# Kernel tuning notes

Hardware: AMD Instinct MI355X
Metric: run time of the kernel (lower is better)

Reference implementation:

```python
import jax, jax.numpy as jnp
import numpy as np

IOU_THRESHOLD = 0.5


def setup_inputs() -> dict:
    key = jax.random.key(0)
    k_xy, k_wh, k_jit, k_cls, k_lab = jax.random.split(key, 5)
    B, P, T, C = 16, 16384, 128, 80
    # valid x1y1x2y2 ground-truth boxes in [0,1]
    xy = jax.random.uniform(k_xy, (B, T, 2), dtype=jnp.float32) * 0.7
    wh = jax.random.uniform(k_wh, (B, T, 2), dtype=jnp.float32) * 0.25 + 0.05
    true_bboxes = jnp.concatenate([xy, xy + wh], axis=-1)  # [B,T,4]
    # predictions: tiled GT boxes + small jitter so many pairs exceed IoU 0.5
    reps = P // T
    base = jnp.tile(true_bboxes, (1, reps, 1))  # [B,P,4]
    pred_bboxes = base + 0.02 * jax.random.normal(k_jit, (B, P, 4), dtype=jnp.float32)
    pred_classes = jax.random.normal(k_cls, (B, P, C), dtype=jnp.float32)
    true_labels = jax.random.randint(k_lab, (B, T), 0, C, dtype=jnp.int64)
    return {
        "pred_bboxes": pred_bboxes,
        "pred_classes": pred_classes,
        "true_bboxes": true_bboxes,
        "true_labels": true_labels,
    }


def _iou_matrix(pred, true):
    # pred [B,P,4], true [B,T,4] -> [B,P,T]
    p = pred[:, :, None, :]  # [B,P,1,4]
    t = true[:, None, :, :]  # [B,1,T,4]
    x1 = jnp.maximum(p[..., 0], t[..., 0])
    y1 = jnp.maximum(p[..., 1], t[..., 1])
    x2 = jnp.minimum(p[..., 2], t[..., 2])
    y2 = jnp.minimum(p[..., 3], t[..., 3])
    inter = jnp.clip(x2 - x1, 0.0) * jnp.clip(y2 - y1, 0.0)
    pa = (pred[..., 2] - pred[..., 0]) * (pred[..., 3] - pred[..., 1])  # [B,P]
    ta = (true[..., 2] - true[..., 0]) * (true[..., 3] - true[..., 1])  # [B,T]
    union = pa[:, :, None] + ta[:, None, :] - inter
    return inter / union


def _smooth_l1(d):
    ad = jnp.abs(d)
    return jnp.where(ad < 1.0, 0.5 * d * d, ad - 0.5)


def reference(pred_bboxes, pred_classes, true_bboxes, true_labels):
    B, P, _ = pred_bboxes.shape
    iou = _iou_matrix(pred_bboxes, true_bboxes)          # [B,P,T]
    max_iou = jnp.max(iou, axis=2)                       # [B,P]
    max_idx = jnp.argmax(iou, axis=2)                    # [B,P]
    matched_true = jnp.take_along_axis(
        true_bboxes, jnp.broadcast_to(max_idx[:, :, None], (B, P, 4)), axis=1
    )                                                    # [B,P,4]
    mask = (max_iou > IOU_THRESHOLD).astype(pred_bboxes.dtype)  # [B,P]
    elem = _smooth_l1(pred_bboxes - matched_true)        # [B,P,4]
    n_matched = jnp.sum(mask)
    bbox_loss = jnp.sum(elem * mask[:, :, None]) / jnp.maximum(4.0 * n_matched, 1.0)
    # classification: per image, first prediction's logits vs first GT label
    logits = pred_classes[:, 0, :]                       # [B,C]
    labels = true_labels[:, 0]                           # [B]
    logp = jax.nn.log_softmax(logits, axis=-1)
    cls_loss = -jnp.mean(jnp.take_along_axis(logp, labels[:, None], axis=1))
    return bbox_loss + cls_loss
```

## Files before the change

kernel.cpp:

```cpp
#include <hip/hip_runtime.h>
#include <hip/hip_bf16.h>
#include <math.h>

#define B_ 16
#define P_ 16384
#define T_ 128
#define C_ 80


__device__ __forceinline__ float smooth_l1(float d) {
    float ad = fabsf(d);
    return (ad < 1.0f) ? 0.5f * d * d : ad - 0.5f;
}

__global__ __launch_bounds__(256) void det_loss_main(
        const float* __restrict__ pred_bboxes,
        const float* __restrict__ true_bboxes,
        float* __restrict__ ws)
{
    const int blocks_per_b = P_ / 512;
    const int b    = blockIdx.x / blocks_per_b;
    const int pblk = blockIdx.x % blocks_per_b;
    const int tid  = threadIdx.x;

    __shared__ float4 tb[T_];
    if (tid < T_) tb[tid] = ((const float4*)true_bboxes)[b * T_ + tid];
    __syncthreads();

    const float4* pbase = (const float4*)pred_bboxes + (size_t)b * P_ + pblk * 512;
    const float4 pA = pbase[tid];
    const float4 pB = pbase[tid + 256];
    const float paA = (pA.z - pA.x) * (pA.w - pA.y);
    const float paB = (pB.z - pB.x) * (pB.w - pB.y);

    float biA = 0.0f, buA = 1.0f; int bxA = 0;
    float biB = 0.0f, buB = 1.0f; int bxB = 0;

    #pragma unroll 8
    for (int t = 0; t < T_; ++t) {
        const float4 t4 = tb[t];
        const float ta = (t4.z - t4.x) * (t4.w - t4.y);

        {
            const float iw = fmaxf(fminf(pA.z, t4.z) - fmaxf(pA.x, t4.x), 0.0f);
            const float ih = fmaxf(fminf(pA.w, t4.w) - fmaxf(pA.y, t4.y), 0.0f);
            const float inter = iw * ih;
            const float u = (paA + ta) - inter;
            const bool upd = inter * buA > biA * u;
            biA = upd ? inter : biA;
            buA = upd ? u : buA;
            bxA = upd ? t : bxA;
        }
        {
            const float iw = fmaxf(fminf(pB.z, t4.z) - fmaxf(pB.x, t4.x), 0.0f);
            const float ih = fmaxf(fminf(pB.w, t4.w) - fmaxf(pB.y, t4.y), 0.0f);
            const float inter = iw * ih;
            const float u = (paB + ta) - inter;
            const bool upd = inter * buB > biB * u;
            biB = upd ? inter : biB;
            buB = upd ? u : buB;
            bxB = upd ? t : bxB;
        }
    }

    float contrib = 0.0f, cnt = 0.0f;
    if (2.0f * biA > buA) {
        const float4 m4 = tb[bxA];
        contrib += smooth_l1(pA.x - m4.x) + smooth_l1(pA.y - m4.y)
                 + smooth_l1(pA.z - m4.z) + smooth_l1(pA.w - m4.w);
        cnt += 1.0f;
    }
    if (2.0f * biB > buB) {
        const float4 m4 = tb[bxB];
        contrib += smooth_l1(pB.x - m4.x) + smooth_l1(pB.y - m4.y)
                 + smooth_l1(pB.z - m4.z) + smooth_l1(pB.w - m4.w);
        cnt += 1.0f;
    }

    #pragma unroll
    for (int off = 32; off > 0; off >>= 1) {
        contrib += __shfl_down(contrib, off, 64);
        cnt     += __shfl_down(cnt,     off, 64);
    }
    __shared__ float sc[4], sn[4];
    const int wave = tid >> 6, lane = tid & 63;
    if (lane == 0) { sc[wave] = contrib; sn[wave] = cnt; }
    __syncthreads();
    if (tid == 0) {
        ws[blockIdx.x]       = sc[0] + sc[1] + sc[2] + sc[3];
        ws[512 + blockIdx.x] = sn[0] + sn[1] + sn[2] + sn[3];
    }
}

__global__ __launch_bounds__(1024) void det_loss_final(
        const float* __restrict__ pred_classes,
        const int*   __restrict__ true_labels,
        const float* __restrict__ ws,
        float* __restrict__ out)
{
    const int tid = threadIdx.x;
    const int wave = tid >> 6, lane = tid & 63;

    __shared__ float rowloss[B_];
    __shared__ float wc[16], wn[16];

    const float* row = pred_classes + (size_t)wave * P_ * C_;
    const float v0 = row[lane];
    const float v1 = (lane < C_ - 64) ? row[lane + 64] : -INFINITY;
    float m = fmaxf(v0, v1);
    #pragma unroll
    for (int off = 32; off > 0; off >>= 1) m = fmaxf(m, __shfl_xor(m, off, 64));
    float s = expf(v0 - m) + ((lane < C_ - 64) ? expf(v1 - m) : 0.0f);
    #pragma unroll
    for (int off = 32; off > 0; off >>= 1) s += __shfl_xor(s, off, 64);
    if (lane == 0) {
        const int lab = true_labels[wave * T_];
        rowloss[wave] = -(row[lab] - m - logf(s));
    }

    float sc = 0.0f, sn = 0.0f;
    if (tid < 128) {
        const float4 c4 = ((const float4*)ws)[tid];
        const float4 n4 = ((const float4*)(ws + 512))[tid];
        sc = c4.x + c4.y + c4.z + c4.w;
        sn = n4.x + n4.y + n4.z + n4.w;
    }
    #pragma unroll
    for (int off = 32; off > 0; off >>= 1) {
        sc += __shfl_down(sc, off, 64);
        sn += __shfl_down(sn, off, 64);
    }
    if (lane == 0) { wc[wave] = sc; wn[wave] = sn; }
    __syncthreads();

    if (tid == 0) {
        float C = 0.0f, N = 0.0f, cl = 0.0f;
        #pragma unroll
        for (int w = 0; w < 16; ++w) { C += wc[w]; N += wn[w]; cl += rowloss[w]; }
        out[0] = C / fmaxf(4.0f * N, 1.0f) + cl * (1.0f / B_);
    }
}

extern "C" void kernel_launch(void* const* d_in, const int* in_sizes, int n_in,
                              void* d_out, int out_size, void* d_ws, size_t ws_size,
                              hipStream_t stream) {
    const float* pred_bboxes  = (const float*)d_in[0];
    const float* pred_classes = (const float*)d_in[1];
    const float* true_bboxes  = (const float*)d_in[2];
    const int*   true_labels  = (const int*)d_in[3];
    float* out = (float*)d_out;
    float* ws  = (float*)d_ws;

    det_loss_main<<<B_ * (P_ / 512), 256, 0, stream>>>(pred_bboxes, true_bboxes, ws);
    det_loss_final<<<1, 1024, 0, stream>>>(pred_classes, true_labels, ws, out);
}
```

Before: 133.5 us.

## Fuse final reduction into main kernel via last-block atomic counter

Merges the two kernels into one. A global atomic counter lets the last finishing block do the final reduction, and the classification log-softmax moves into one wave of each image's first block. Ground-truth boxes are now read straight from global memory as scalar loads instead of being staged in LDS. The IoU comparison now tracks pa+ta instead of the union, with the threshold rewritten as 3*inter > sum. This removes a kernel launch and one LDS barrier, at the cost of a memset launch and an atomic/threadfence per block.

Result: slower. 141.3 us (+5.9%).

```diff
diff --git a/kernel.cpp b/kernel.cpp
--- a/kernel.cpp
+++ b/kernel.cpp
@@ -6,6 +6,7 @@
 #define P_ 16384
 #define T_ 128
 #define C_ 80
+#define NBLK 512
 
 
 __device__ __forceinline__ float smooth_l1(float d) {
@@ -13,19 +14,20 @@
     return (ad < 1.0f) ? 0.5f * d * d : ad - 0.5f;
 }
 
-__global__ __launch_bounds__(256) void det_loss_main(
+__global__ __launch_bounds__(256) void det_loss_fused(
         const float* __restrict__ pred_bboxes,
+        const float* __restrict__ pred_classes,
         const float* __restrict__ true_bboxes,
-        float* __restrict__ ws)
+        const int*   __restrict__ true_labels,
+        float* __restrict__ ws,
+        float* __restrict__ out)
 {
-    const int blocks_per_b = P_ / 512;
-    const int b    = blockIdx.x / blocks_per_b;
-    const int pblk = blockIdx.x % blocks_per_b;
     const int tid  = threadIdx.x;
+    const int b    = blockIdx.x >> 5;
+    const int pblk = blockIdx.x & 31;
+    const int wave = tid >> 6, lane = tid & 63;
 
-    __shared__ float4 tb[T_];
-    if (tid < T_) tb[tid] = ((const float4*)true_bboxes)[b * T_ + tid];
-    __syncthreads();
+    const float* tb = true_bboxes + b * (T_ * 4);
 
     const float4* pbase = (const float4*)pred_bboxes + (size_t)b * P_ + pblk * 512;
     const float4 pA = pbase[tid];
@@ -33,48 +35,66 @@
     const float paA = (pA.z - pA.x) * (pA.w - pA.y);
     const float paB = (pB.z - pB.x) * (pB.w - pB.y);
 
-    float biA = 0.0f, buA = 1.0f; int bxA = 0;
-    float biB = 0.0f, buB = 1.0f; int bxB = 0;
+    float biA = 0.0f, bsA = 1.0f; int bxA = 0;
+    float biB = 0.0f, bsB = 1.0f; int bxB = 0;
 
     #pragma unroll 8
     for (int t = 0; t < T_; ++t) {
-        const float4 t4 = tb[t];
-        const float ta = (t4.z - t4.x) * (t4.w - t4.y);
-
+        const float tx = tb[4 * t + 0];
+        const float ty = tb[4 * t + 1];
+        const float tz = tb[4 * t + 2];
+        const float tw = tb[4 * t + 3];
+        const float ta = (tz - tx) * (tw - ty);
+        const float sA = paA + ta;
+        const float sB = paB + ta;
         {
-            const float iw = fmaxf(fminf(pA.z, t4.z) - fmaxf(pA.x, t4.x), 0.0f);
-            const float ih = fmaxf(fminf(pA.w, t4.w) - fmaxf(pA.y, t4.y), 0.0f);
+            const float iw = fmaxf(fminf(pA.z, tz) - fmaxf(pA.x, tx), 0.0f);
+            const float ih = fmaxf(fminf(pA.w, tw) - fmaxf(pA.y, ty), 0.0f);
             const float inter = iw * ih;
-            const float u = (paA + ta) - inter;
-            const bool upd = inter * buA > biA * u;
+            const bool upd = inter * bsA > biA * sA;
             biA = upd ? inter : biA;
-            buA = upd ? u : buA;
+            bsA = upd ? sA : bsA;
             bxA = upd ? t : bxA;
         }
         {
-            const float iw = fmaxf(fminf(pB.z, t4.z) - fmaxf(pB.x, t4.x), 0.0f);
-            const float ih = fmaxf(fminf(pB.w, t4.w) - fmaxf(pB.y, t4.y), 0.0f);
+            const float iw = fmaxf(fminf(pB.z, tz) - fmaxf(pB.x, tx), 0.0f);
+            const float ih = fmaxf(fminf(pB.w, tw) - fmaxf(pB.y, ty), 0.0f);
             const float inter = iw * ih;
-            const float u = (paB + ta) - inter;
-            const bool upd = inter * buB > biB * u;
+            const bool upd = inter * bsB > biB * sB;
             biB = upd ? inter : biB;
-            buB = upd ? u : buB;
+            bsB = upd ? sB : bsB;
             bxB = upd ? t : bxB;
         }
     }
 
     float contrib = 0.0f, cnt = 0.0f;
-    if (2.0f * biA > buA) {
-        const float4 m4 = tb[bxA];
+    if (3.0f * biA > bsA) {
+        const float4 m4 = ((const float4*)tb)[bxA];
         contrib += smooth_l1(pA.x - m4.x) + smooth_l1(pA.y - m4.y)
                  + smooth_l1(pA.z - m4.z) + smooth_l1(pA.w - m4.w);
         cnt += 1.0f;
     }
-    if (2.0f * biB > buB) {
-        const float4 m4 = tb[bxB];
+    if (3.0f * biB > bsB) {
+        const float4 m4 = ((const float4*)tb)[bxB];
         contrib += smooth_l1(pB.x - m4.x) + smooth_l1(pB.y - m4.y)
                  + smooth_l1(pB.z - m4.z) + smooth_l1(pB.w - m4.w);
         cnt += 1.0f;
+    }
+
+    if (pblk == 0 && wave == 0) {
+        const float* row = pred_classes + (size_t)b * (P_ * C_);
+        const float v0 = row[lane];
+        const float v1 = (lane < C_ - 64) ? row[lane + 64] : -INFINITY;
+        float m = fmaxf(v0, v1);
+        #pragma unroll
+        for (int off = 32; off > 0; off >>= 1) m = fmaxf(m, __shfl_xor(m, off, 64));
+        float s = expf(v0 - m) + ((lane < C_ - 64) ? expf(v1 - m) : 0.0f);
+        #pragma unroll
+        for (int off = 32; off > 0; off >>= 1) s += __shfl_xor(s, off, 64);
+        if (lane == 0) {
+            const int lab = true_labels[b * T_];
+            ws[1024 + b] = -(row[lab] - m - logf(s));
+        }
     }
 
     #pragma unroll
@@ -83,61 +103,44 @@
         cnt     += __shfl_down(cnt,     off, 64);
     }
     __shared__ float sc[4], sn[4];
-    const int wave = tid >> 6, lane = tid & 63;
+    __shared__ int isLast;
     if (lane == 0) { sc[wave] = contrib; sn[wave] = cnt; }
     __syncthreads();
     if (tid == 0) {
-        ws[blockIdx.x]       = sc[0] + sc[1] + sc[2] + sc[3];
-        ws[512 + blockIdx.x] = sn[0] + sn[1] + sn[2] + sn[3];
+        ws[blockIdx.x]        = sc[0] + sc[1] + sc[2] + sc[3];
+        ws[512 + blockIdx.x]  = sn[0] + sn[1] + sn[2] + sn[3];
+        __threadfence();
+        unsigned old = atomicAdd((unsigned*)(ws + 1056), 1u);
+        isLast = (old == NBLK - 1);
     }
-}
+    __syncthreads();
+    if (!isLast) return;
 
-__global__ __launch_bounds__(1024) void det_loss_final(
-        const float* __restrict__ pred_classes,
-        const int*   __restrict__ true_labels,
-        const float* __restrict__ ws,
-        float* __restrict__ out)
-{
-    const int tid = threadIdx.x;
-    const int wave = tid >> 6, lane = tid & 63;
-
-    __shared__ float rowloss[B_];
-    __shared__ float wc[16], wn[16];
-
-    const float* row = pred_classes + (size_t)wave * P_ * C_;
-    const float v0 = row[lane];
-    const float v1 = (lane < C_ - 64) ? row[lane + 64] : -INFINITY;
-    float m = fmaxf(v0, v1);
-    #pragma unroll
-    for (int off = 32; off > 0; off >>= 1) m = fmaxf(m, __shfl_xor(m, off, 64));
-    float s = expf(v0 - m) + ((lane < C_ - 64) ? expf(v1 - m) : 0.0f);
-    #pragma unroll
-    for (int off = 32; off > 0; off >>= 1) s += __shfl_xor(s, off, 64);
-    if (lane == 0) {
-        const int lab = true_labels[wave * T_];
-        rowloss[wave] = -(row[lab] - m - logf(s));
-    }
-
-    float sc = 0.0f, sn = 0.0f;
+    __threadfence();
+    float fc = 0.0f, fn = 0.0f;
     if (tid < 128) {
         const float4 c4 = ((const float4*)ws)[tid];
         const float4 n4 = ((const float4*)(ws + 512))[tid];
-        sc = c4.x + c4.y + c4.z + c4.w;
-        sn = n4.x + n4.y + n4.z + n4.w;
+        fc = c4.x + c4.y + c4.z + c4.w;
+        fn = n4.x + n4.y + n4.z + n4.w;
     }
     #pragma unroll
     for (int off = 32; off > 0; off >>= 1) {
-        sc += __shfl_down(sc, off, 64);
-        sn += __shfl_down(sn, off, 64);
+        fc += __shfl_down(fc, off, 64);
+        fn += __shfl_down(fn, off, 64);
     }
-    if (lane == 0) { wc[wave] = sc; wn[wave] = sn; }
+    float cl = (tid < 16) ? ws[1024 + tid] : 0.0f;
+    #pragma unroll
+    for (int off = 8; off > 0; off >>= 1) cl += __shfl_down(cl, off, 64);
+
+    __shared__ float wc[4], wn[4], wcl;
+    if (lane == 0) { wc[wave] = fc; wn[wave] = fn; }
+    if (tid == 0) wcl = cl;
     __syncthreads();
-
     if (tid == 0) {
-        float C = 0.0f, N = 0.0f, cl = 0.0f;
-        #pragma unroll
-        for (int w = 0; w < 16; ++w) { C += wc[w]; N += wn[w]; cl += rowloss[w]; }
-        out[0] = C / fmaxf(4.0f * N, 1.0f) + cl * (1.0f / B_);
+        const float C = wc[0] + wc[1] + wc[2] + wc[3];
+        const float N = wn[0] + wn[1] + wn[2] + wn[3];
+        out[0] = C / fmaxf(4.0f * N, 1.0f) + wcl * (1.0f / B_);
     }
 }
 
@@ -151,6 +154,8 @@
     float* out = (float*)d_out;
     float* ws  = (float*)d_ws;
 
-    det_loss_main<<<B_ * (P_ / 512), 256, 0, stream>>>(pred_bboxes, true_bboxes, ws);
-    det_loss_final<<<1, 1024, 0, stream>>>(pred_classes, true_labels, ws, out);
+    hipMemsetAsync((char*)d_ws + 1056 * sizeof(float), 0, 4, stream);
+
+    det_loss_fused<<<NBLK, 256, 0, stream>>>(pred_bboxes, pred_classes,
+                                             true_bboxes, true_labels, ws, out);
 }
```
